# Kernel tuning notes

Measured on AMD Instinct MI355X. Metric: run time of the kernel, lower is better.

## Reference

```python
import jax, jax.numpy as jnp
import numpy as np
import math

N = 2048       # num_nodes (dense graph)
F_IN = 256     # num_in_features
F_OUT = 256    # num_out_features
H = 8          # num_heads
LN_EPS = 1e-5

# NOTE: every e3nn FullyConnectedTensorProduct in this module maps
# (Fx0e) x irreps_sh -> (Kx0e). Only the l=0 spherical-harmonic component can
# couple scalars to scalars, and Y_0 = 1 under normalization='component'.
# Each TP is therefore exactly a linear map with a 1/sqrt(fan_in) path norm,
# and edge_direction does not enter the math at all.


def setup_inputs() -> dict:
    key = jax.random.key(0)
    ks = jax.random.split(key, 12)
    inv = 1.0 / np.sqrt(F_IN)
    return {
        "node_features": jax.random.normal(ks[0], (N, F_IN), jnp.float32),
        "edges_features_distance": jax.random.uniform(ks[1], (N, N), jnp.float32),
        "edges_features_bond": jax.random.uniform(ks[2], (N, N), jnp.float32),
        "edge_direction": jax.random.normal(ks[3], (N * N, 3), jnp.float32),
        "degree_matrix": jax.random.randint(ks[4], (N, N), 0, 2).astype(jnp.float32),
        # tensor-product weights (xavier-ish scale)
        "Wq": jax.random.normal(ks[5], (F_IN, H), jnp.float32) * inv,
        "Wk": jax.random.normal(ks[6], (F_IN, H), jnp.float32) * inv,
        "Wv": jax.random.normal(ks[7], (F_IN, F_OUT), jnp.float32) * inv,
        "w_bond": jax.random.normal(ks[8], (), jnp.float32),
        "w_bond_contrib": jax.random.normal(ks[9], (), jnp.float32),
        "w_gauss": jax.random.normal(ks[10], (), jnp.float32),
    }


def reference(node_features, edges_features_distance, edges_features_bond,
              edge_direction, degree_matrix, Wq, Wk, Wv,
              w_bond, w_bond_contrib, w_gauss):
    scale = 1.0 / jnp.sqrt(jnp.asarray(F_IN, node_features.dtype))
    # scalar-only tensor products == scaled linears (Y_0 = 1)
    q = (node_features @ Wq) * scale              # [N, H]
    k = (node_features @ Wk) * scale              # [N, H]
    v = (node_features @ Wv) * scale              # [N, F_OUT]

    # raw_attention[i,j,h] = (q_i + k_i)/sqrt(H)  (key.transpose(0,1) picks node i)
    qk = (q + k) / math.sqrt(H)                   # [N, H]
    bond = edges_features_bond * (w_bond * w_bond_contrib)   # [N, N]
    gauss = edges_features_distance * w_gauss                 # [N, N]
    raw = qk[:, None, :] + (bond + gauss)[:, :, None]          # [N, N, H]

    mask = jnp.where(degree_matrix > 0, 0.0, -1e9).astype(raw.dtype)
    scores = jax.nn.leaky_relu(raw, 0.2) + mask[:, :, None]
    # torch F.softmax without dim on a 3-D tensor -> dim=0
    attn = jax.nn.softmax(scores, axis=0)          # [N, N, H]
    # F.dropout treated as identity (eval / deterministic baseline)
    attn_mean = attn.mean(axis=2)                  # [N, N]

    # aggregated[i] = sum_j attn_mean[i,j] * v_j  (value[i,j,:] = v(node_j))
    aggregated = attn_mean @ v                     # [N, F_OUT]
    updated_nodes = jax.nn.elu(aggregated)

    # no_grad connectivity update
    un = jax.lax.stop_gradient(updated_nodes)
    sim = un @ un.T                                # [N, N]
    dd = -jax.lax.stop_gradient(edges_features_distance)
    conn = jax.nn.sigmoid(sim) * dd * jax.lax.stop_gradient(degree_matrix)
    mu = conn.mean(axis=-1, keepdims=True)
    var = conn.var(axis=-1, keepdims=True)
    conn = (conn - mu) * jax.lax.rsqrt(var + LN_EPS)
    conn = conn + conn.T
    return updated_nodes, conn
```

## Files before the change

kernel.cpp:

```cpp
#include <hip/hip_runtime.h>
#include <hip/hip_bf16.h>

#define NN 2048
#define FIN 256
#define FOUT 256
#define HH 8

__global__ __launch_bounds__(256) void k1_qkv(
    const float* __restrict__ x, const float* __restrict__ Wq,
    const float* __restrict__ Wk, const float* __restrict__ Wv,
    float* __restrict__ v, float* __restrict__ qk)
{
    const int ib = blockIdx.x * 2;
    const int t  = threadIdx.x;
    __shared__ float xs[2][FIN];
    __shared__ float part[128];
    xs[0][t] = x[(long)ib*FIN + t];
    xs[1][t] = x[(long)(ib+1)*FIN + t];
    __syncthreads();
    float a0 = 0.f, a1 = 0.f;
    #pragma unroll 8
    for (int c = 0; c < FIN; ++c) {
        const float w = Wv[c*FOUT + t];
        a0 = fmaf(xs[0][c], w, a0);
        a1 = fmaf(xs[1][c], w, a1);
    }
    v[ib*FOUT + t]     = a0 * 0.0625f;
    v[(ib+1)*FOUT + t] = a1 * 0.0625f;
    if (t < 128) {
        const int n = t >> 6, h = t & 7, seg = (t >> 3) & 7;
        float a = 0.f;
        for (int c = seg*32; c < seg*32 + 32; ++c)
            a = fmaf(xs[n][c], Wq[c*HH + h] + Wk[c*HH + h], a);
        part[t] = a;
    }
    __syncthreads();
    if (t < 16) {
        const int n = t >> 3, h = t & 7;
        float a = 0.f;
        #pragma unroll
        for (int s2 = 0; s2 < 8; ++s2) a += part[n*64 + s2*8 + h];
        qk[(ib+n)*HH + h] = a * (0.0625f * 0.35355339059327373f);
    }
}

__global__ __launch_bounds__(256) void k2_denom(
    const float* __restrict__ bond, const float* __restrict__ dist,
    const float* __restrict__ deg, const float* __restrict__ qk,
    const float* __restrict__ wb, const float* __restrict__ wbc,
    const float* __restrict__ wg, float* __restrict__ D)
{
    const float cb = wb[0] * wbc[0];
    const float cg = wg[0];
    const int tx = threadIdx.x & 63, ty = threadIdx.x >> 6;
    const int j  = blockIdx.x * 64 + tx;
    const int i0 = blockIdx.y * 128;
    __shared__ float qs[128*8];
    for (int p = threadIdx.x; p < 128*8; p += 256) qs[p] = qk[i0*8 + p];
    __syncthreads();
    float acc[8];
    #pragma unroll
    for (int h = 0; h < 8; ++h) acc[h] = 0.f;
    for (int ii = ty; ii < 128; ii += 4) {
        const long idx = (long)(i0 + ii)*NN + j;
        const float m = (deg[idx] > 0.f) ? 1.f : 0.f;
        const float s = fmaf(cb, bond[idx], cg * dist[idx]);
        #pragma unroll
        for (int h = 0; h < 8; ++h) {
            float r = qs[ii*8 + h] + s;
            r = (r > 0.f) ? r : 0.2f*r;
            acc[h] += m * __expf(r);
        }
    }
    __shared__ float red[4][64][8];
    #pragma unroll
    for (int h = 0; h < 8; ++h) red[ty][tx][h] = acc[h];
    __syncthreads();
    for (int p = threadIdx.x; p < 512; p += 256) {
        const int jj = p >> 3, h = p & 7;
        const float ssum = red[0][jj][h] + red[1][jj][h] + red[2][jj][h] + red[3][jj][h];
        atomicAdd(&D[(blockIdx.x*64 + jj)*8 + h], ssum);
    }
}

__global__ __launch_bounds__(256) void k3_attnmean(
    const float* __restrict__ bond, const float* __restrict__ dist,
    const float* __restrict__ deg, const float* __restrict__ qk,
    const float* __restrict__ wb, const float* __restrict__ wbc,
    const float* __restrict__ wg, const float* __restrict__ D,
    float* __restrict__ am)
{
    const float cb = wb[0] * wbc[0];
    const float cg = wg[0];
    const int tx = threadIdx.x & 63, ty = threadIdx.x >> 6;
    const int j  = blockIdx.x * 64 + tx;
    const int i0 = blockIdx.y * 128;
    __shared__ float qs[128*8];
    for (int p = threadIdx.x; p < 128*8; p += 256) qs[p] = qk[i0*8 + p];
    __syncthreads();
    float invD[8];
    #pragma unroll
    for (int h = 0; h < 8; ++h) invD[h] = 1.f / fmaxf(D[j*8 + h], 1e-30f);
    for (int ii = ty; ii < 128; ii += 4) {
        const long idx = (long)(i0 + ii)*NN + j;
        const float m = (deg[idx] > 0.f) ? 0.125f : 0.f;
        const float s = fmaf(cb, bond[idx], cg * dist[idx]);
        float o = 0.f;
        #pragma unroll
        for (int h = 0; h < 8; ++h) {
            float r = qs[ii*8 + h] + s;
            r = (r > 0.f) ? r : 0.2f*r;
            o = fmaf(__expf(r), invD[h], o);
        }
        am[idx] = o * m;
    }
}

__global__ __launch_bounds__(256) void k4_aggr(
    const float* __restrict__ am, const float* __restrict__ v,
    float* __restrict__ partial)
{
    const int i0 = blockIdx.x * 64;
    const int f0 = blockIdx.y * 64;
    const int k0 = blockIdx.z * 256;
    const int t  = threadIdx.x;
    const int tx = t & 15, ty = t >> 4;
    __shared__ float Ast[16][68];
    __shared__ float Bs [16][68];
    float acc[4][4];
    #pragma unroll
    for (int r = 0; r < 4; ++r)
        #pragma unroll
        for (int c = 0; c < 4; ++c) acc[r][c] = 0.f;

    const int lr = t >> 2;
    const int lc = (t & 3) * 4;
    const int vr = t >> 4;
    const int vc = (t & 15) * 4;

    for (int kk = k0; kk < k0 + 256; kk += 16) {
        const float4 a4 = *(const float4*)&am[(long)(i0 + lr)*NN + kk + lc];
        const float4 b4 = *(const float4*)&v[(kk + vr)*FOUT + f0 + vc];
        Ast[lc+0][lr] = a4.x; Ast[lc+1][lr] = a4.y;
        Ast[lc+2][lr] = a4.z; Ast[lc+3][lr] = a4.w;
        *(float4*)&Bs[vr][vc] = b4;
        __syncthreads();
        #pragma unroll
        for (int k2 = 0; k2 < 16; ++k2) {
            const float4 av = *(const float4*)&Ast[k2][ty*4];
            const float4 bv = *(const float4*)&Bs[k2][tx*4];
            const float a[4] = {av.x, av.y, av.z, av.w};
            const float b[4] = {bv.x, bv.y, bv.z, bv.w};
            #pragma unroll
            for (int r = 0; r < 4; ++r)
                #pragma unroll
                for (int c = 0; c < 4; ++c)
                    acc[r][c] = fmaf(a[r], b[c], acc[r][c]);
        }
        __syncthreads();
    }
    float* out = partial + (long)blockIdx.z * NN * FOUT;
    #pragma unroll
    for (int r = 0; r < 4; ++r)
        *(float4*)&out[(i0 + ty*4 + r)*FOUT + f0 + tx*4] = *(float4*)&acc[r][0];
}

__global__ __launch_bounds__(256) void k4b_elu(
    const float* __restrict__ partial, float* __restrict__ un)
{
    const int idx = blockIdx.x*256 + threadIdx.x;
    const float4* p = (const float4*)partial;
    float4 s = p[idx];
    #pragma unroll
    for (int z = 1; z < 8; ++z) {
        const float4 q = p[idx + z*(NN*FOUT/4)];
        s.x += q.x; s.y += q.y; s.z += q.z; s.w += q.w;
    }
    s.x = (s.x > 0.f) ? s.x : (__expf(s.x) - 1.f);
    s.y = (s.y > 0.f) ? s.y : (__expf(s.y) - 1.f);
    s.z = (s.z > 0.f) ? s.z : (__expf(s.z) - 1.f);
    s.w = (s.w > 0.f) ? s.w : (__expf(s.w) - 1.f);
    ((float4*)un)[idx] = s;
}

__global__ __launch_bounds__(256) void k5_sim(
    const float* __restrict__ un, const float* __restrict__ dist,
    const float* __restrict__ deg, float* __restrict__ c0,
    float* __restrict__ rowsum, float* __restrict__ rowsq)
{
    const int i0 = blockIdx.y * 64;
    const int j0 = blockIdx.x * 64;
    const int t  = threadIdx.x;
    const int tx = t & 15, ty = t >> 4;
    __shared__ float As[16][68];
    __shared__ float Bs[16][68];
    float acc[4][4];
    #pragma unroll
    for (int r = 0; r < 4; ++r)
        #pragma unroll
        for (int c = 0; c < 4; ++c) acc[r][c] = 0.f;

    const int lr = t >> 2;
    const int lc = (t & 3) * 4;

    for (int kk = 0; kk < FOUT; kk += 16) {
        const float4 a4 = *(const float4*)&un[(i0 + lr)*FOUT + kk + lc];
        const float4 b4 = *(const float4*)&un[(j0 + lr)*FOUT + kk + lc];
        As[lc+0][lr] = a4.x; As[lc+1][lr] = a4.y;
        As[lc+2][lr] = a4.z; As[lc+3][lr] = a4.w;
        Bs[lc+0][lr] = b4.x; Bs[lc+1][lr] = b4.y;
        Bs[lc+2][lr] = b4.z; Bs[lc+3][lr] = b4.w;
        __syncthreads();
        #pragma unroll
        for (int k2 = 0; k2 < 16; ++k2) {
            const float4 av = *(const float4*)&As[k2][ty*4];
            const float4 bv = *(const float4*)&Bs[k2][tx*4];
            const float a[4] = {av.x, av.y, av.z, av.w};
            const float b[4] = {bv.x, bv.y, bv.z, bv.w};
            #pragma unroll
            for (int r = 0; r < 4; ++r)
                #pragma unroll
                for (int c = 0; c < 4; ++c)
                    acc[r][c] = fmaf(a[r], b[c], acc[r][c]);
        }
        __syncthreads();
    }
    #pragma unroll
    for (int r = 0; r < 4; ++r) {
        const int i = i0 + ty*4 + r;
        const long rb = (long)i*NN + j0 + tx*4;
        const float4 d4 = *(const float4*)&dist[rb];
        const float4 g4 = *(const float4*)&deg[rb];
        const float dd[4] = {d4.x, d4.y, d4.z, d4.w};
        const float gg[4] = {g4.x, g4.y, g4.z, g4.w};
        float val[4];
        float srow = 0.f, qrow = 0.f;
        #pragma unroll
        for (int c = 0; c < 4; ++c) {
            const float sg = 1.f / (1.f + __expf(-acc[r][c]));
            val[c] = sg * (-dd[c]) * gg[c];
            srow += val[c];
            qrow = fmaf(val[c], val[c], qrow);
        }
        *(float4*)&c0[rb] = *(float4*)&val[0];
        #pragma unroll
        for (int off = 8; off > 0; off >>= 1) {
            srow += __shfl_down(srow, off, 16);
            qrow += __shfl_down(qrow, off, 16);
        }
        if (tx == 0) {
            atomicAdd(&rowsum[i], srow);
            atomicAdd(&rowsq[i],  qrow);
        }
    }
}

__global__ void k6_stats(const float* __restrict__ rowsum,
                         const float* __restrict__ rowsq,
                         float* __restrict__ mu, float* __restrict__ rs)
{
    const int i = blockIdx.x*256 + threadIdx.x;
    if (i < NN) {
        const float m = rowsum[i] * (1.f/NN);
        const float var = rowsq[i] * (1.f/NN) - m*m;
        mu[i] = m;
        rs[i] = rsqrtf(var + 1e-5f);
    }
}

__global__ __launch_bounds__(256) void k7_conn(
    const float* __restrict__ c0, const float* __restrict__ mu,
    const float* __restrict__ rs, float* __restrict__ out1)
{
    const int i0 = blockIdx.y * 64;
    const int j0 = blockIdx.x * 64;
    const int t  = threadIdx.x;
    __shared__ float L[64][65];
    #pragma unroll
    for (int p = 0; p < 16; ++p) {
        const int lid = t + p*256;
        const int a = lid >> 6, b = lid & 63;
        L[a][b] = c0[(long)(j0 + a)*NN + i0 + b];
    }
    __syncthreads();
    #pragma unroll
    for (int p = 0; p < 16; ++p) {
        const int lid = t + p*256;
        const int rr = lid >> 6, cc = lid & 63;
        const int i = i0 + rr, j = j0 + cc;
        const float x  = c0[(long)i*NN + j];
        const float xt = L[cc][rr];
        out1[(long)i*NN + j] = (x - mu[i])*rs[i] + (xt - mu[j])*rs[j];
    }
}

extern "C" void kernel_launch(void* const* d_in, const int* in_sizes, int n_in,
                              void* d_out, int out_size, void* d_ws, size_t ws_size,
                              hipStream_t stream)
{
    const float* x    = (const float*)d_in[0];
    const float* dist = (const float*)d_in[1];
    const float* bond = (const float*)d_in[2];
    const float* deg  = (const float*)d_in[4];
    const float* Wq   = (const float*)d_in[5];
    const float* Wk   = (const float*)d_in[6];
    const float* Wv   = (const float*)d_in[7];
    const float* wb   = (const float*)d_in[8];
    const float* wbc  = (const float*)d_in[9];
    const float* wg   = (const float*)d_in[10];

    float* out0 = (float*)d_out;
    float* out1 = out0 + (size_t)NN*FOUT;

    char* w = (char*)d_ws;
    float* am      = (float*)(w);
    float* partial = (float*)(w + 16777216);
    float* v       = (float*)(w + 33554432);
    float* qk      = (float*)(w + 35651584);
    float* D       = (float*)(w + 35717120);
    float* rowsum  = (float*)(w + 35782656);
    float* rowsq   = (float*)(w + 35790848);
    float* mu      = (float*)(w + 35799040);
    float* rs      = (float*)(w + 35807232);

    hipMemsetAsync(D, 0, 65536 + 8192 + 8192, stream);

    k1_qkv<<<NN/2, 256, 0, stream>>>(x, Wq, Wk, Wv, v, qk);
    dim3 g23(NN/64, NN/128);
    k2_denom<<<g23, 256, 0, stream>>>(bond, dist, deg, qk, wb, wbc, wg, D);
    k3_attnmean<<<g23, 256, 0, stream>>>(bond, dist, deg, qk, wb, wbc, wg, D, am);
    dim3 g4(NN/64, FOUT/64, 8);
    k4_aggr<<<g4, 256, 0, stream>>>(am, v, partial);
    k4b_elu<<<NN*FOUT/4/256, 256, 0, stream>>>(partial, out0);
    dim3 g5(NN/64, NN/64);
    k5_sim<<<g5, 256, 0, stream>>>(out0 , dist, deg, am , rowsum, rowsq);
    k6_stats<<<8, 256, 0, stream>>>(rowsum, rowsq, mu, rs);
    k7_conn<<<g5, 256, 0, stream>>>(am, mu, rs, out1);
}
```

Before: 267.0 us.

## Move both GEMMs to bf16 MFMA and cache masked edge score in bf16

The attention-aggregation and similarity GEMMs now run on bf16 MFMA instructions instead of scalar FP32 FMAs, with a new kernel that transposes v into bf16. The denominator kernel writes a masked bf16 edge score that the attention-mean kernel reuses, so it no longer rereads bond, dist and deg, and the attention matrix is stored in bf16. Also included: 4 rows per block in the QKV kernel, fewer split-K partials, and a vectorised transpose in the connectivity kernel. The aim is to cut memory traffic and ALU time, at the cost of bf16 rounding in the attention weights and similarity inputs.

```diff
diff --git a/kernel.cpp b/kernel.cpp
--- a/kernel.cpp
+++ b/kernel.cpp
@@ -6,28 +6,42 @@
 #define FOUT 256
 #define HH 8
 
+typedef short bhalf8 __attribute__((ext_vector_type(8)));
+typedef float f32x4  __attribute__((ext_vector_type(4)));
+
+__device__ __forceinline__ unsigned short f2b(float f) {
+    __hip_bfloat16 h = __float2bfloat16(f);
+    return *reinterpret_cast<unsigned short*>(&h);
+}
+__device__ __forceinline__ float b2f(unsigned short u) {
+    __hip_bfloat16 h = *reinterpret_cast<__hip_bfloat16*>(&u);
+    return __bfloat162float(h);
+}
+
 __global__ __launch_bounds__(256) void k1_qkv(
     const float* __restrict__ x, const float* __restrict__ Wq,
     const float* __restrict__ Wk, const float* __restrict__ Wv,
     float* __restrict__ v, float* __restrict__ qk)
 {
-    const int ib = blockIdx.x * 2;
+    const int ib = blockIdx.x * 4;
     const int t  = threadIdx.x;
-    __shared__ float xs[2][FIN];
-    __shared__ float part[128];
-    xs[0][t] = x[(long)ib*FIN + t];
-    xs[1][t] = x[(long)(ib+1)*FIN + t];
-    __syncthreads();
-    float a0 = 0.f, a1 = 0.f;
-    #pragma unroll 8
+    __shared__ float xs[4][FIN];
+    __shared__ float part[256];
+    #pragma unroll
+    for (int n = 0; n < 4; ++n) xs[n][t] = x[(long)(ib+n)*FIN + t];
+    __syncthreads();
+    float a0 = 0.f, a1 = 0.f, a2 = 0.f, a3 = 0.f;
+    #pragma unroll 4
     for (int c = 0; c < FIN; ++c) {
-        const float w = Wv[c*FOUT + t];
-        a0 = fmaf(xs[0][c], w, a0);
-        a1 = fmaf(xs[1][c], w, a1);
-    }
-    v[ib*FOUT + t]     = a0 * 0.0625f;
+        const float wv = Wv[c*FOUT + t];
+        a0 = fmaf(xs[0][c], wv, a0); a1 = fmaf(xs[1][c], wv, a1);
+        a2 = fmaf(xs[2][c], wv, a2); a3 = fmaf(xs[3][c], wv, a3);
+    }
+    v[(ib+0)*FOUT + t] = a0 * 0.0625f;
     v[(ib+1)*FOUT + t] = a1 * 0.0625f;
-    if (t < 128) {
+    v[(ib+2)*FOUT + t] = a2 * 0.0625f;
+    v[(ib+3)*FOUT + t] = a3 * 0.0625f;
+    {
         const int n = t >> 6, h = t & 7, seg = (t >> 3) & 7;
         float a = 0.f;
         for (int c = seg*32; c < seg*32 + 32; ++c)
@@ -35,12 +49,38 @@
         part[t] = a;
     }
     __syncthreads();
-    if (t < 16) {
+    if (t < 32) {
         const int n = t >> 3, h = t & 7;
         float a = 0.f;
         #pragma unroll
         for (int s2 = 0; s2 < 8; ++s2) a += part[n*64 + s2*8 + h];
         qk[(ib+n)*HH + h] = a * (0.0625f * 0.35355339059327373f);
+    }
+}
+
+__global__ __launch_bounds__(256) void k1b_vT(
+    const float* __restrict__ v, unsigned short* __restrict__ vtb)
+{
+    const int k0 = blockIdx.x * 64;
+    const int f0 = blockIdx.y * 64;
+    const int t  = threadIdx.x;
+    __shared__ float LT[64][68];
+    const int r  = t >> 4;
+    const int c4 = (t & 15) * 4;
+    #pragma unroll
+    for (int p = 0; p < 4; ++p) {
+        const float4 q = *(const float4*)&v[(k0 + r + p*16)*FOUT + f0 + c4];
+        LT[c4+0][r + p*16] = q.x; LT[c4+1][r + p*16] = q.y;
+        LT[c4+2][r + p*16] = q.z; LT[c4+3][r + p*16] = q.w;
+    }
+    __syncthreads();
+    #pragma unroll
+    for (int p = 0; p < 4; ++p) {
+        const int fr = r + p*16;
+        ushort4 ub;
+        ub.x = f2b(LT[fr][c4+0]); ub.y = f2b(LT[fr][c4+1]);
+        ub.z = f2b(LT[fr][c4+2]); ub.w = f2b(LT[fr][c4+3]);
+        *(ushort4*)&vtb[(long)(f0 + fr)*NN + k0 + c4] = ub;
     }
 }
 
@@ -48,7 +88,8 @@
     const float* __restrict__ bond, const float* __restrict__ dist,
     const float* __restrict__ deg, const float* __restrict__ qk,
     const float* __restrict__ wb, const float* __restrict__ wbc,
-    const float* __restrict__ wg, float* __restrict__ D)
+    const float* __restrict__ wg, float* __restrict__ D,
+    unsigned short* __restrict__ fbuf)
 {
     const float cb = wb[0] * wbc[0];
     const float cg = wg[0];
@@ -63,13 +104,15 @@
     for (int h = 0; h < 8; ++h) acc[h] = 0.f;
     for (int ii = ty; ii < 128; ii += 4) {
         const long idx = (long)(i0 + ii)*NN + j;
-        const float m = (deg[idx] > 0.f) ? 1.f : 0.f;
-        const float s = fmaf(cb, bond[idx], cg * dist[idx]);
+        const float s0 = fmaf(cb, bond[idx], cg * dist[idx]);
+        const unsigned short fb = f2b((deg[idx] > 0.f) ? s0 : -__builtin_inff());
+        fbuf[idx] = fb;
+        const float s = b2f(fb);
         #pragma unroll
         for (int h = 0; h < 8; ++h) {
             float r = qs[ii*8 + h] + s;
             r = (r > 0.f) ? r : 0.2f*r;
-            acc[h] += m * __expf(r);
+            acc[h] += __expf(r);
         }
     }
     __shared__ float red[4][64][8];
@@ -84,14 +127,9 @@
 }
 
 __global__ __launch_bounds__(256) void k3_attnmean(
-    const float* __restrict__ bond, const float* __restrict__ dist,
-    const float* __restrict__ deg, const float* __restrict__ qk,
-    const float* __restrict__ wb, const float* __restrict__ wbc,
-    const float* __restrict__ wg, const float* __restrict__ D,
-    float* __restrict__ am)
-{
-    const float cb = wb[0] * wbc[0];
-    const float cg = wg[0];
+    const unsigned short* __restrict__ fbuf, const float* __restrict__ qk,
+    const float* __restrict__ D, unsigned short* __restrict__ amb)
+{
     const int tx = threadIdx.x & 63, ty = threadIdx.x >> 6;
     const int j  = blockIdx.x * 64 + tx;
     const int i0 = blockIdx.y * 128;
@@ -100,11 +138,10 @@
     __syncthreads();
     float invD[8];
     #pragma unroll
-    for (int h = 0; h < 8; ++h) invD[h] = 1.f / fmaxf(D[j*8 + h], 1e-30f);
+    for (int h = 0; h < 8; ++h) invD[h] = 0.125f / fmaxf(D[j*8 + h], 1e-30f);
     for (int ii = ty; ii < 128; ii += 4) {
         const long idx = (long)(i0 + ii)*NN + j;
-        const float m = (deg[idx] > 0.f) ? 0.125f : 0.f;
-        const float s = fmaf(cb, bond[idx], cg * dist[idx]);
+        const float s = b2f(fbuf[idx]);
         float o = 0.f;
         #pragma unroll
         for (int h = 0; h < 8; ++h) {
@@ -112,67 +149,47 @@
             r = (r > 0.f) ? r : 0.2f*r;
             o = fmaf(__expf(r), invD[h], o);
         }
-        am[idx] = o * m;
+        amb[idx] = f2b(o);
     }
 }
 
 __global__ __launch_bounds__(256) void k4_aggr(
-    const float* __restrict__ am, const float* __restrict__ v,
-    float* __restrict__ partial)
+    const unsigned short* __restrict__ amb,
+    const unsigned short* __restrict__ vtb, float* __restrict__ partial)
 {
     const int i0 = blockIdx.x * 64;
     const int f0 = blockIdx.y * 64;
-    const int k0 = blockIdx.z * 256;
-    const int t  = threadIdx.x;
-    const int tx = t & 15, ty = t >> 4;
-    __shared__ float Ast[16][68];
-    __shared__ float Bs [16][68];
-    float acc[4][4];
-    #pragma unroll
-    for (int r = 0; r < 4; ++r)
-        #pragma unroll
-        for (int c = 0; c < 4; ++c) acc[r][c] = 0.f;
-
-    const int lr = t >> 2;
-    const int lc = (t & 3) * 4;
-    const int vr = t >> 4;
-    const int vc = (t & 15) * 4;
-
-    for (int kk = k0; kk < k0 + 256; kk += 16) {
-        const float4 a4 = *(const float4*)&am[(long)(i0 + lr)*NN + kk + lc];
-        const float4 b4 = *(const float4*)&v[(kk + vr)*FOUT + f0 + vc];
-        Ast[lc+0][lr] = a4.x; Ast[lc+1][lr] = a4.y;
-        Ast[lc+2][lr] = a4.z; Ast[lc+3][lr] = a4.w;
-        *(float4*)&Bs[vr][vc] = b4;
-        __syncthreads();
-        #pragma unroll
-        for (int k2 = 0; k2 < 16; ++k2) {
-            const float4 av = *(const float4*)&Ast[k2][ty*4];
-            const float4 bv = *(const float4*)&Bs[k2][tx*4];
-            const float a[4] = {av.x, av.y, av.z, av.w};
-            const float b[4] = {bv.x, bv.y, bv.z, bv.w};
-            #pragma unroll
-            for (int r = 0; r < 4; ++r)
-                #pragma unroll
-                for (int c = 0; c < 4; ++c)
-                    acc[r][c] = fmaf(a[r], b[c], acc[r][c]);
-        }
-        __syncthreads();
+    const int k0 = blockIdx.z * 512;
+    const int w  = threadIdx.x >> 6;
+    const int l  = threadIdx.x & 63;
+    const int lm = l & 15, lq = l >> 4;
+    const int iw = i0 + w*16;
+    f32x4 acc[4] = {f32x4{0,0,0,0}, f32x4{0,0,0,0}, f32x4{0,0,0,0}, f32x4{0,0,0,0}};
+    for (int kk = k0; kk < k0 + 512; kk += 32) {
+        const bhalf8 a = *(const bhalf8*)&amb[(long)(iw + lm)*NN + kk + lq*8];
+        #pragma unroll
+        for (int c = 0; c < 4; ++c) {
+            const bhalf8 b = *(const bhalf8*)&vtb[(long)(f0 + c*16 + lm)*NN + kk + lq*8];
+            acc[c] = __builtin_amdgcn_mfma_f32_16x16x32_bf16(a, b, acc[c], 0, 0, 0);
+        }
     }
     float* out = partial + (long)blockIdx.z * NN * FOUT;
     #pragma unroll
-    for (int r = 0; r < 4; ++r)
-        *(float4*)&out[(i0 + ty*4 + r)*FOUT + f0 + tx*4] = *(float4*)&acc[r][0];
+    for (int c = 0; c < 4; ++c)
+        #pragma unroll
+        for (int r = 0; r < 4; ++r)
+            out[(iw + lq*4 + r)*FOUT + f0 + c*16 + lm] = acc[c][r];
 }
 
 __global__ __launch_bounds__(256) void k4b_elu(
-    const float* __restrict__ partial, float* __restrict__ un)
+    const float* __restrict__ partial, float* __restrict__ un,
+    unsigned short* __restrict__ unb)
 {
     const int idx = blockIdx.x*256 + threadIdx.x;
     const float4* p = (const float4*)partial;
     float4 s = p[idx];
     #pragma unroll
-    for (int z = 1; z < 8; ++z) {
+    for (int z = 1; z < 4; ++z) {
         const float4 q = p[idx + z*(NN*FOUT/4)];
         s.x += q.x; s.y += q.y; s.z += q.z; s.w += q.w;
     }
@@ -181,76 +198,55 @@
     s.z = (s.z > 0.f) ? s.z : (__expf(s.z) - 1.f);
     s.w = (s.w > 0.f) ? s.w : (__expf(s.w) - 1.f);
     ((float4*)un)[idx] = s;
+    ushort4 ub; ub.x = f2b(s.x); ub.y = f2b(s.y); ub.z = f2b(s.z); ub.w = f2b(s.w);
+    *(ushort4*)&unb[(long)idx*4] = ub;
 }
 
 __global__ __launch_bounds__(256) void k5_sim(
-    const float* __restrict__ un, const float* __restrict__ dist,
+    const unsigned short* __restrict__ unb, const float* __restrict__ dist,
     const float* __restrict__ deg, float* __restrict__ c0,
     float* __restrict__ rowsum, float* __restrict__ rowsq)
 {
     const int i0 = blockIdx.y * 64;
     const int j0 = blockIdx.x * 64;
-    const int t  = threadIdx.x;
-    const int tx = t & 15, ty = t >> 4;
-    __shared__ float As[16][68];
-    __shared__ float Bs[16][68];
-    float acc[4][4];
-    #pragma unroll
-    for (int r = 0; r < 4; ++r)
-        #pragma unroll
-        for (int c = 0; c < 4; ++c) acc[r][c] = 0.f;
-
-    const int lr = t >> 2;
-    const int lc = (t & 3) * 4;
-
-    for (int kk = 0; kk < FOUT; kk += 16) {
-        const float4 a4 = *(const float4*)&un[(i0 + lr)*FOUT + kk + lc];
-        const float4 b4 = *(const float4*)&un[(j0 + lr)*FOUT + kk + lc];
-        As[lc+0][lr] = a4.x; As[lc+1][lr] = a4.y;
-        As[lc+2][lr] = a4.z; As[lc+3][lr] = a4.w;
-        Bs[lc+0][lr] = b4.x; Bs[lc+1][lr] = b4.y;
-        Bs[lc+2][lr] = b4.z; Bs[lc+3][lr] = b4.w;
-        __syncthreads();
-        #pragma unroll
-        for (int k2 = 0; k2 < 16; ++k2) {
-            const float4 av = *(const float4*)&As[k2][ty*4];
-            const float4 bv = *(const float4*)&Bs[k2][tx*4];
-            const float a[4] = {av.x, av.y, av.z, av.w};
-            const float b[4] = {bv.x, bv.y, bv.z, bv.w};
-            #pragma unroll
-            for (int r = 0; r < 4; ++r)
-                #pragma unroll
-                for (int c = 0; c < 4; ++c)
-                    acc[r][c] = fmaf(a[r], b[c], acc[r][c]);
-        }
-        __syncthreads();
+    const int w  = threadIdx.x >> 6;
+    const int l  = threadIdx.x & 63;
+    const int lm = l & 15, lq = l >> 4;
+    const int iw = i0 + w*16;
+    f32x4 acc[4] = {f32x4{0,0,0,0}, f32x4{0,0,0,0}, f32x4{0,0,0,0}, f32x4{0,0,0,0}};
+    for (int kk = 0; kk < FOUT; kk += 32) {
+        const bhalf8 a = *(const bhalf8*)&unb[(long)(iw + lm)*FOUT + kk + lq*8];
+        #pragma unroll
+        for (int c = 0; c < 4; ++c) {
+            const bhalf8 b = *(const bhalf8*)&unb[(long)(j0 + c*16 + lm)*FOUT + kk + lq*8];
+            acc[c] = __builtin_amdgcn_mfma_f32_16x16x32_bf16(a, b, acc[c], 0, 0, 0);
+        }
+    }
+    float srow[4] = {0.f,0.f,0.f,0.f}, qrow[4] = {0.f,0.f,0.f,0.f};
+    #pragma unroll
+    for (int c = 0; c < 4; ++c) {
+        #pragma unroll
+        for (int r = 0; r < 4; ++r) {
+            const int i = iw + lq*4 + r;
+            const int j = j0 + c*16 + lm;
+            const long idx = (long)i*NN + j;
+            const float sg = 1.f / (1.f + __expf(-acc[c][r]));
+            const float val = sg * (-dist[idx]) * deg[idx];
+            c0[idx] = val;
+            srow[r] += val;
+            qrow[r] = fmaf(val, val, qrow[r]);
+        }
     }
     #pragma unroll
     for (int r = 0; r < 4; ++r) {
-        const int i = i0 + ty*4 + r;
-        const long rb = (long)i*NN + j0 + tx*4;
-        const float4 d4 = *(const float4*)&dist[rb];
-        const float4 g4 = *(const float4*)&deg[rb];
-        const float dd[4] = {d4.x, d4.y, d4.z, d4.w};
-        const float gg[4] = {g4.x, g4.y, g4.z, g4.w};
-        float val[4];
-        float srow = 0.f, qrow = 0.f;
-        #pragma unroll
-        for (int c = 0; c < 4; ++c) {
-            const float sg = 1.f / (1.f + __expf(-acc[r][c]));
-            val[c] = sg * (-dd[c]) * gg[c];
-            srow += val[c];
-            qrow = fmaf(val[c], val[c], qrow);
-        }
-        *(float4*)&c0[rb] = *(float4*)&val[0];
-        #pragma unroll
-        for (int off = 8; off > 0; off >>= 1) {
-            srow += __shfl_down(srow, off, 16);
-            qrow += __shfl_down(qrow, off, 16);
-        }
-        if (tx == 0) {
-            atomicAdd(&rowsum[i], srow);
-            atomicAdd(&rowsq[i],  qrow);
+        #pragma unroll
+        for (int m = 8; m >= 1; m >>= 1) {
+            srow[r] += __shfl_xor(srow[r], m, 64);
+            qrow[r] += __shfl_xor(qrow[r], m, 64);
+        }
+        if (lm == 0) {
+            atomicAdd(&rowsum[iw + lq*4 + r], srow[r]);
+            atomicAdd(&rowsq[iw + lq*4 + r],  qrow[r]);
         }
     }
 }
@@ -275,22 +271,33 @@
     const int i0 = blockIdx.y * 64;
     const int j0 = blockIdx.x * 64;
     const int t  = threadIdx.x;
-    __shared__ float L[64][65];
-    #pragma unroll
-    for (int p = 0; p < 16; ++p) {
-        const int lid = t + p*256;
-        const int a = lid >> 6, b = lid & 63;
-        L[a][b] = c0[(long)(j0 + a)*NN + i0 + b];
-    }
-    __syncthreads();
-    #pragma unroll
-    for (int p = 0; p < 16; ++p) {
-        const int lid = t + p*256;
-        const int rr = lid >> 6, cc = lid & 63;
-        const int i = i0 + rr, j = j0 + cc;
-        const float x  = c0[(long)i*NN + j];
-        const float xt = L[cc][rr];
-        out1[(long)i*NN + j] = (x - mu[i])*rs[i] + (xt - mu[j])*rs[j];
+    __shared__ float LT[64][68];
+    __shared__ float muj[64], rsj[64];
+    const int r  = t >> 4;
+    const int c4 = (t & 15) * 4;
+    if (t < 64)        muj[t] = mu[j0 + t];
+    else if (t < 128)  rsj[t-64] = rs[j0 + t - 64];
+    #pragma unroll
+    for (int p = 0; p < 4; ++p) {
+        const int jl = r + p*16;
+        const float4 q = *(const float4*)&c0[(long)(j0 + jl)*NN + i0 + c4];
+        LT[c4+0][jl] = q.x; LT[c4+1][jl] = q.y;
+        LT[c4+2][jl] = q.z; LT[c4+3][jl] = q.w;
+    }
+    __syncthreads();
+    #pragma unroll
+    for (int p = 0; p < 4; ++p) {
+        const int rr = r + p*16;
+        const int i  = i0 + rr;
+        const float4 x = *(const float4*)&c0[(long)i*NN + j0 + c4];
+        const float4 xt = *(const float4*)&LT[rr][c4];
+        const float mi = mu[i], ri = rs[i];
+        float4 o;
+        o.x = (x.x - mi)*ri + (xt.x - muj[c4+0])*rsj[c4+0];
+        o.y = (x.y - mi)*ri + (xt.y - muj[c4+1])*rsj[c4+1];
+        o.z = (x.z - mi)*ri + (xt.z - muj[c4+2])*rsj[c4+2];
+        o.w = (x.w - mi)*ri + (xt.w - muj[c4+3])*rsj[c4+3];
+        *(float4*)&out1[(long)i*NN + j0 + c4] = o;
     }
 }
 
@@ -313,27 +320,33 @@
     float* out1 = out0 + (size_t)NN*FOUT;
 
     char* w = (char*)d_ws;
-    float* am      = (float*)(w);
+    unsigned short* fbuf = (unsigned short*)(w);
+    unsigned short* amb  = (unsigned short*)(w + 8388608);
+    float* c0      = (float*)(w);
     float* partial = (float*)(w + 16777216);
-    float* v       = (float*)(w + 33554432);
-    float* qk      = (float*)(w + 35651584);
-    float* D       = (float*)(w + 35717120);
-    float* rowsum  = (float*)(w + 35782656);
-    float* rowsq   = (float*)(w + 35790848);
-    float* mu      = (float*)(w + 35799040);
-    float* rs      = (float*)(w + 35807232);
+    float* v       = (float*)(w + 25165824);
+    unsigned short* vtb = (unsigned short*)(w + 27262976);
+    unsigned short* unb = (unsigned short*)(w + 28311552);
+    float* qk      = (float*)(w + 29360128);
+    float* D       = (float*)(w + 29425664);
+    float* rowsum  = (float*)(w + 29491200);
+    float* rowsq   = (float*)(w + 29499392);
+    float* mu      = (float*)(w + 29507584);
+    float* rs      = (float*)(w + 29515776);
 
     hipMemsetAsync(D, 0, 65536 + 8192 + 8192, stream);
 
-    k1_qkv<<<NN/2, 256, 0, stream>>>(x, Wq, Wk, Wv, v, qk);
+    k1_qkv<<<NN/4, 256, 0, stream>>>(x, Wq, Wk, Wv, v, qk);
+    dim3 g1b(NN/64, FOUT/64);
+    k1b_vT<<<g1b, 256, 0, stream>>>(v, vtb);
     dim3 g23(NN/64, NN/128);
-    k2_denom<<<g23, 256, 0, stream>>>(bond, dist, deg, qk, wb, wbc, wg, D);
-    k3_attnmean<<<g23, 256, 0, stream>>>(bond, dist, deg, qk, wb, wbc, wg, D, am);
-    dim3 g4(NN/64, FOUT/64, 8);
-    k4_aggr<<<g4, 256, 0, stream>>>(am, v, partial);
-    k4b_elu<<<NN*FOUT/4/256, 256, 0, stream>>>(partial, out0);
+    k2_denom<<<g23, 256, 0, stream>>>(bond, dist, deg, qk, wb, wbc, wg, D, fbuf);
+    k3_attnmean<<<g23, 256, 0, stream>>>(fbuf, qk, D, amb);
+    dim3 g4(NN/64, FOUT/64, 4);
+    k4_aggr<<<g4, 256, 0, stream>>>(amb, vtb, partial);
+    k4b_elu<<<NN*FOUT/4/256, 256, 0, stream>>>(partial, out0, unb);
     dim3 g5(NN/64, NN/64);
-    k5_sim<<<g5, 256, 0, stream>>>(out0 , dist, deg, am , rowsum, rowsq);
+    k5_sim<<<g5, 256, 0, stream>>>(unb, dist, deg, c0, rowsum, rowsq);
     k6_stats<<<8, 256, 0, stream>>>(rowsum, rowsq, mu, rs);
-    k7_conn<<<g5, 256, 0, stream>>>(am, mu, rs, out1);
-}
+    k7_conn<<<g5, 256, 0, stream>>>(c0, mu, rs, out1);
+}
```

Measured after the change: 260.2 us. 1.03x faster.
